# Kernel optimization log

Hardware: AMD Instinct MI355X
Metric: run time of the kernel (lower is better)

The kernel has to match this reference:

```python
import jax, jax.numpy as jnp
import numpy as np

NEG_SLOPE = 0.2
EPS = 1e-16  # PyG softmax denominator epsilon


def gat_conv(x, src, dst, W, a_src, a_dst, bias, concat):
    """PyG-style GATConv (eval mode, self-loops already included in src/dst)."""
    H, D = a_src.shape
    N = x.shape[0]
    h = (x @ W).reshape(N, H, D)                     # [N,H,D]
    alpha_s = jnp.einsum('nhd,hd->nh', h, a_src)     # [N,H]
    alpha_d = jnp.einsum('nhd,hd->nh', h, a_dst)     # [N,H]
    e = alpha_s[src] + alpha_d[dst]                  # [E,H]
    e = jax.nn.leaky_relu(e, NEG_SLOPE)
    # segment softmax over destination nodes
    m = jax.ops.segment_max(e, dst, num_segments=N)  # [N,H]
    m = jax.lax.stop_gradient(m)
    w = jnp.exp(e - m[dst])                          # [E,H]
    denom = jax.ops.segment_sum(w, dst, num_segments=N)  # [N,H]
    a = w / (denom[dst] + EPS)                       # [E,H]
    msg = h[src] * a[:, :, None]                     # [E,H,D]
    out = jax.ops.segment_sum(msg, dst, num_segments=N)  # [N,H,D]
    out = out.reshape(N, H * D) if concat else out.mean(axis=1)
    return out + bias


def setup_inputs() -> dict:
    key = jax.random.key(0)
    ks = jax.random.split(key, 10)
    N, E = 50000, 800000
    F_IN, H, D, C = 256, 4, 64, 64
    HID = H * D  # 256
    x = jax.random.normal(ks[0], (N, F_IN), dtype=jnp.float32)
    edge_index = jax.random.randint(ks[1], (2, E), 0, N, dtype=jnp.int64)
    g = 1.0 / np.sqrt(F_IN)
    W0 = jax.random.normal(ks[2], (F_IN, HID), dtype=jnp.float32) * g
    att_src0 = jax.random.normal(ks[3], (H, D), dtype=jnp.float32) * 0.1
    att_dst0 = jax.random.normal(ks[4], (H, D), dtype=jnp.float32) * 0.1
    b0 = jnp.zeros((HID,), dtype=jnp.float32)
    g2 = 1.0 / np.sqrt(HID)
    W1 = jax.random.normal(ks[5], (HID, C), dtype=jnp.float32) * g2
    att_src1 = jax.random.normal(ks[6], (1, C), dtype=jnp.float32) * 0.1
    att_dst1 = jax.random.normal(ks[7], (1, C), dtype=jnp.float32) * 0.1
    b1 = jnp.zeros((C,), dtype=jnp.float32)
    return {"x": x, "edge_index": edge_index, "W0": W0, "att_src0": att_src0,
            "att_dst0": att_dst0, "b0": b0, "W1": W1, "att_src1": att_src1,
            "att_dst1": att_dst1, "b1": b1}


def reference(x, edge_index, W0, att_src0, att_dst0, b0, W1, att_src1, att_dst1, b1):
    N = x.shape[0]
    loops = jnp.arange(N, dtype=edge_index.dtype)
    src = jnp.concatenate([edge_index[0], loops])  # add self-loops (PyG default)
    dst = jnp.concatenate([edge_index[1], loops])
    # layer 0: concat heads, then ELU (dropout is identity in eval mode)
    h = gat_conv(x, src, dst, W0, att_src0, att_dst0, b0, concat=True)
    h = jax.nn.elu(h)
    # layer 1: single head, no concat (mean over 1 head)
    out = gat_conv(h, src, dst, W1, att_src1, att_dst1, b1, concat=False)
    return out
```

## Files before the change

kernel.cpp:

```cpp
#include <hip/hip_runtime.h>
#include <hip/hip_bf16.h>
#include <math.h>


#define NEG_SLOPE 0.2f
#define CAP0 128
#define CAP1 128

typedef __attribute__((ext_vector_type(8))) short bf16x8;
typedef __attribute__((ext_vector_type(4))) float f32x4;

static __device__ __forceinline__ unsigned f2bf_rne(float f) {
  unsigned u = __float_as_uint(f);
  return (u + 0x7fffu + ((u >> 16) & 1u)) >> 16;
}
static __device__ __forceinline__ float bf2f(unsigned u16) {
  return __uint_as_float(u16 << 16);
}
static __device__ __forceinline__ void fma4(float4& acc, float w, uint2 v) {
  acc.x = fmaf(w, __uint_as_float(v.x << 16), acc.x);
  acc.y = fmaf(w, __uint_as_float(v.x & 0xffff0000u), acc.y);
  acc.z = fmaf(w, __uint_as_float(v.y << 16), acc.z);
  acc.w = fmaf(w, __uint_as_float(v.y & 0xffff0000u), acc.w);
}


__global__ void gat_cvt_bf16(const float* __restrict__ in,
                             ushort* __restrict__ out, int n8) {
  int i = blockIdx.x * blockDim.x + threadIdx.x;
  if (i >= n8) return;
  float4 a = *(const float4*)&in[(size_t)i * 8];
  float4 b = *(const float4*)&in[(size_t)i * 8 + 4];
  uint4 o;
  o.x = f2bf_rne(a.x) | (f2bf_rne(a.y) << 16);
  o.y = f2bf_rne(a.z) | (f2bf_rne(a.w) << 16);
  o.z = f2bf_rne(b.x) | (f2bf_rne(b.y) << 16);
  o.w = f2bf_rne(b.z) | (f2bf_rne(b.w) << 16);
  *(uint4*)&out[(size_t)i * 8] = o;
}

__global__ void gat_cvtT_bf16(const float* __restrict__ W,
                              ushort* __restrict__ Wt, int K, int Nw) {
  int i = blockIdx.x * blockDim.x + threadIdx.x;
  if (i >= K * Nw) return;
  int n = i / K, k = i - n * K;
  Wt[i] = (ushort)f2bf_rne(W[(size_t)k * Nw + n]);
}


__global__ void gat_count_kernel(const int* __restrict__ dst, int E, int N,
                                 int* __restrict__ counts) {
  int i = blockIdx.x * blockDim.x + threadIdx.x;
  int ET = E + N;
  if (i >= ET) return;
  int d = (i < E) ? dst[i] : (i - E);
  atomicAdd(&counts[d], 1);
}

__global__ __launch_bounds__(1024) void gat_scan_kernel(
    const int* __restrict__ counts, int* __restrict__ row_off,
    int* __restrict__ cursor, int n) {
  __shared__ int wsum[16];
  __shared__ int s_carry;
  int tid = threadIdx.x;
  int lane = tid & 63;
  int wid = tid >> 6;
  if (tid == 0) s_carry = 0;
  __syncthreads();
  const int TILE = 4096;
  for (int base = 0; base < n; base += TILE) {
    int idx = base + tid * 4;
    int4 v = {0, 0, 0, 0};
    if (idx + 3 < n) {
      v = *(const int4*)&counts[idx];
    } else {
      if (idx + 0 < n) v.x = counts[idx + 0];
      if (idx + 1 < n) v.y = counts[idx + 1];
      if (idx + 2 < n) v.z = counts[idx + 2];
      if (idx + 3 < n) v.w = counts[idx + 3];
    }
    int t0 = v.x, t1 = t0 + v.y, t2 = t1 + v.z, t3 = t2 + v.w;
    int x = t3;
    #pragma unroll
    for (int off = 1; off < 64; off <<= 1) {
      int y = __shfl_up(x, off, 64);
      if (lane >= off) x += y;
    }
    if (lane == 63) wsum[wid] = x;
    __syncthreads();
    if (tid < 16) {
      int s = wsum[tid];
      #pragma unroll
      for (int off = 1; off < 16; off <<= 1) {
        int y = __shfl_up(s, off, 16);
        if (tid >= off) s += y;
      }
      wsum[tid] = s;
    }
    __syncthreads();
    int carry = s_carry;
    int excl_wave = (wid > 0) ? wsum[wid - 1] : 0;
    int b = carry + excl_wave + (x - t3);
    if (idx + 0 < n) { row_off[idx + 0] = b;      cursor[idx + 0] = b;      }
    if (idx + 1 < n) { row_off[idx + 1] = b + t0; cursor[idx + 1] = b + t0; }
    if (idx + 2 < n) { row_off[idx + 2] = b + t1; cursor[idx + 2] = b + t1; }
    if (idx + 3 < n) { row_off[idx + 3] = b + t2; cursor[idx + 3] = b + t2; }
    __syncthreads();
    if (tid == 1023) s_carry = b + t3;
    __syncthreads();
  }
  if (threadIdx.x == 0) row_off[n] = s_carry;
}

__global__ void gat_fill_kernel(const int* __restrict__ src,
                                const int* __restrict__ dst, int E, int N,
                                int* __restrict__ cursor, int* __restrict__ col) {
  int i = blockIdx.x * blockDim.x + threadIdx.x;
  int ET = E + N;
  if (i >= ET) return;
  int s, d;
  if (i < E) { s = src[i]; d = dst[i]; }
  else       { s = d = i - E; }
  int pos = atomicAdd(&cursor[d], 1);
  col[pos] = s;
}


template <int BN, int WM, int WN, bool WRITE_F32, bool WRITE_BF16, bool ALPHA>
__global__ __launch_bounds__(256) void gat_gemm_bf16(
    const ushort* __restrict__ A, const ushort* __restrict__ Bt,
    float* __restrict__ C, ushort* __restrict__ Cb, int M, int K, int N,
    const float* __restrict__ a_src, const float* __restrict__ a_dst,
    float* __restrict__ as_out, float* __restrict__ ad_out, int H) {
  constexpr int BM = 128, BK = 32;
  constexpr int MR = WM / 16, NR = WN / 16;
  constexpr int WCOLS = BN / WN;
  __shared__ __align__(16) ushort Al[BM][40];
  __shared__ __align__(16) ushort Bl[BN][40];
  int tid = threadIdx.x;
  int lane = tid & 63, wid = tid >> 6;
  int wrow = (wid / WCOLS) * WM, wcol = (wid % WCOLS) * WN;
  int brow = blockIdx.x * BM, bcol = blockIdx.y * BN;
  int r0 = tid >> 2, seg = tid & 3;
  int kg = lane >> 4, rl = lane & 15;
  f32x4 acc[MR][NR] = {};
  for (int k0 = 0; k0 < K; k0 += BK) {
    #pragma unroll
    for (int h = 0; h < BM / 64; ++h) {
      int row = r0 + h * 64;
      int ar = brow + row;
      uint4 v = make_uint4(0u, 0u, 0u, 0u);
      if (ar < M) v = *(const uint4*)&A[(size_t)ar * K + k0 + seg * 8];
      *(uint4*)&Al[row][seg * 8] = v;
    }
    #pragma unroll
    for (int h = 0; h < BN / 64; ++h) {
      int row = r0 + h * 64;
      uint4 v = *(const uint4*)&Bt[(size_t)(bcol + row) * K + k0 + seg * 8];
      *(uint4*)&Bl[row][seg * 8] = v;
    }
    __syncthreads();
    bf16x8 af[MR], bfr[NR];
    #pragma unroll
    for (int m = 0; m < MR; ++m)
      af[m] = *(const bf16x8*)&Al[wrow + m * 16 + rl][kg * 8];
    #pragma unroll
    for (int n = 0; n < NR; ++n)
      bfr[n] = *(const bf16x8*)&Bl[wcol + n * 16 + rl][kg * 8];
    #pragma unroll
    for (int m = 0; m < MR; ++m)
      #pragma unroll
      for (int n = 0; n < NR; ++n)
        acc[m][n] = __builtin_amdgcn_mfma_f32_16x16x32_bf16(
            af[m], bfr[n], acc[m][n], 0, 0, 0);
    __syncthreads();
  }
  int orow = kg * 4;
  #pragma unroll
  for (int m = 0; m < MR; ++m) {
    #pragma unroll
    for (int j = 0; j < 4; ++j) {
      int r = brow + wrow + m * 16 + orow + j;
      if (r < M) {
        #pragma unroll
        for (int n = 0; n < NR; ++n) {
          int c = bcol + wcol + n * 16 + rl;
          float v = acc[m][n][j];
          if constexpr (WRITE_F32) C[(size_t)r * N + c] = v;
          if constexpr (WRITE_BF16) Cb[(size_t)r * N + c] = (ushort)f2bf_rne(v);
        }
      }
    }
  }
  if constexpr (ALPHA) {
    static_assert(WN == 64, "alpha fusion needs one head per wave");
    int hh = (bcol + wcol) >> 6;
    float asv[NR], adv[NR];
    #pragma unroll
    for (int n = 0; n < NR; ++n) {
      asv[n] = a_src[hh * 64 + n * 16 + rl];
      adv[n] = a_dst[hh * 64 + n * 16 + rl];
    }
    #pragma unroll
    for (int m = 0; m < MR; ++m) {
      #pragma unroll
      for (int j = 0; j < 4; ++j) {
        float ps = 0.f, pd = 0.f;
        #pragma unroll
        for (int n = 0; n < NR; ++n) {
          ps = fmaf(acc[m][n][j], asv[n], ps);
          pd = fmaf(acc[m][n][j], adv[n], pd);
        }
        #pragma unroll
        for (int off = 1; off < 16; off <<= 1) {
          ps += __shfl_xor(ps, off, 64);
          pd += __shfl_xor(pd, off, 64);
        }
        int r = brow + wrow + m * 16 + orow + j;
        if (rl == 0 && r < M) {
          as_out[(size_t)r * H + hh] = ps;
          ad_out[(size_t)r * H + hh] = pd;
        }
      }
    }
  }
}


__global__ __launch_bounds__(256) void gat_agg0_kernel(
    const unsigned* __restrict__ h0b, const float* __restrict__ as,
    const float* __restrict__ ad, const int* __restrict__ row_off,
    const int* __restrict__ col, const float* __restrict__ bias,
    ushort* __restrict__ x1b, int N) {
  __shared__ int scol[4][CAP0];
  __shared__ float wt[4][CAP0][4];
  int lane = threadIdx.x & 63;
  int wid = threadIdx.x >> 6;
  int n = blockIdx.x * 4 + wid;
  if (n >= N) return;
  int beg = row_off[n];
  int deg = row_off[n + 1] - beg;
  int degc = deg < CAP0 ? deg : CAP0;
  for (int jj = lane; jj < degc; jj += 64) scol[wid][jj] = col[beg + jj];

  int q = lane >> 4, slot = lane & 15;
  float adv = ad[n * 4 + q];

  float m = -INFINITY;
  for (int jj = slot; jj < deg; jj += 16) {
    int s = (jj < CAP0) ? scol[wid][jj] : col[beg + jj];
    float e = as[s * 4 + q] + adv;
    e = (e > 0.f) ? e : NEG_SLOPE * e;
    if (jj < CAP0) wt[wid][jj][q] = e;
    m = fmaxf(m, e);
  }
  #pragma unroll
  for (int off = 8; off; off >>= 1) m = fmaxf(m, __shfl_xor(m, off, 64));

  float dsum = 0.f;
  for (int jj = slot; jj < deg; jj += 16) {
    float e;
    if (jj < CAP0) {
      e = wt[wid][jj][q];
    } else {
      int s = col[beg + jj];
      e = as[s * 4 + q] + adv;
      e = (e > 0.f) ? e : NEG_SLOPE * e;
    }
    float w = __expf(e - m);
    if (jj < CAP0) wt[wid][jj][q] = w;
    dsum += w;
  }
  #pragma unroll
  for (int off = 8; off; off >>= 1) dsum += __shfl_xor(dsum, off, 64);
  float inv = 1.f / (dsum + 1e-16f);

  float4 acc = make_float4(0.f, 0.f, 0.f, 0.f);
  int c2 = lane * 2;
  if (deg <= CAP0) {
    int jj = 0;
    for (; jj + 8 <= deg; jj += 8) {
      int s0 = __builtin_amdgcn_readfirstlane(scol[wid][jj + 0]);
      int s1 = __builtin_amdgcn_readfirstlane(scol[wid][jj + 1]);
      int s2 = __builtin_amdgcn_readfirstlane(scol[wid][jj + 2]);
      int s3 = __builtin_amdgcn_readfirstlane(scol[wid][jj + 3]);
      int s4 = __builtin_amdgcn_readfirstlane(scol[wid][jj + 4]);
      int s5 = __builtin_amdgcn_readfirstlane(scol[wid][jj + 5]);
      int s6 = __builtin_amdgcn_readfirstlane(scol[wid][jj + 6]);
      int s7 = __builtin_amdgcn_readfirstlane(scol[wid][jj + 7]);
      uint2 v0 = *(const uint2*)(h0b + (size_t)s0 * 128 + c2);
      uint2 v1 = *(const uint2*)(h0b + (size_t)s1 * 128 + c2);
      uint2 v2 = *(const uint2*)(h0b + (size_t)s2 * 128 + c2);
      uint2 v3 = *(const uint2*)(h0b + (size_t)s3 * 128 + c2);
      uint2 v4 = *(const uint2*)(h0b + (size_t)s4 * 128 + c2);
      uint2 v5 = *(const uint2*)(h0b + (size_t)s5 * 128 + c2);
      uint2 v6 = *(const uint2*)(h0b + (size_t)s6 * 128 + c2);
      uint2 v7 = *(const uint2*)(h0b + (size_t)s7 * 128 + c2);
      float w0 = wt[wid][jj + 0][q];
      float w1 = wt[wid][jj + 1][q];
      float w2 = wt[wid][jj + 2][q];
      float w3 = wt[wid][jj + 3][q];
      float w4 = wt[wid][jj + 4][q];
      float w5 = wt[wid][jj + 5][q];
      float w6 = wt[wid][jj + 6][q];
      float w7 = wt[wid][jj + 7][q];
      fma4(acc, w0, v0); fma4(acc, w1, v1); fma4(acc, w2, v2); fma4(acc, w3, v3);
      fma4(acc, w4, v4); fma4(acc, w5, v5); fma4(acc, w6, v6); fma4(acc, w7, v7);
    }
    for (; jj < deg; ++jj) {
      int s = __builtin_amdgcn_readfirstlane(scol[wid][jj]);
      uint2 v = *(const uint2*)(h0b + (size_t)s * 128 + c2);
      fma4(acc, wt[wid][jj][q], v);
    }
  } else {
    for (int jj = 0; jj < deg; ++jj) {
      int s = (jj < CAP0) ? scol[wid][jj] : col[beg + jj];
      s = __builtin_amdgcn_readfirstlane(s);
      uint2 v = *(const uint2*)(h0b + (size_t)s * 128 + c2);
      float w;
      if (jj < CAP0) {
        w = wt[wid][jj][q];
      } else {
        float e = as[s * 4 + q] + adv;
        e = (e > 0.f) ? e : NEG_SLOPE * e;
        w = __expf(e - m);
      }
      fma4(acc, w, v);
    }
  }

  int c0 = lane * 4;
  float4 bv = *(const float4*)&bias[c0];
  float o0 = acc.x * inv + bv.x;
  float o1 = acc.y * inv + bv.y;
  float o2 = acc.z * inv + bv.z;
  float o3 = acc.w * inv + bv.w;
  o0 = (o0 > 0.f) ? o0 : (__expf(o0) - 1.f);
  o1 = (o1 > 0.f) ? o1 : (__expf(o1) - 1.f);
  o2 = (o2 > 0.f) ? o2 : (__expf(o2) - 1.f);
  o3 = (o3 > 0.f) ? o3 : (__expf(o3) - 1.f);
  uint2 p;
  p.x = f2bf_rne(o0) | (f2bf_rne(o1) << 16);
  p.y = f2bf_rne(o2) | (f2bf_rne(o3) << 16);
  *(uint2*)&x1b[(size_t)n * 256 + c0] = p;
}


__global__ __launch_bounds__(256) void gat_agg1_kernel(
    const ushort* __restrict__ h1b, const float* __restrict__ as,
    const float* __restrict__ ad, const int* __restrict__ row_off,
    const int* __restrict__ col, const float* __restrict__ bias,
    float* __restrict__ out, int N) {
  __shared__ int scol[4][CAP1];
  __shared__ float wt[4][CAP1];
  int lane = threadIdx.x & 63;
  int wid = threadIdx.x >> 6;
  int n = blockIdx.x * 4 + wid;
  if (n >= N) return;
  int beg = row_off[n];
  int deg = row_off[n + 1] - beg;
  int degc = deg < CAP1 ? deg : CAP1;
  for (int jj = lane; jj < degc; jj += 64) scol[wid][jj] = col[beg + jj];
  float adv = ad[n];

  float m = -INFINITY;
  for (int jj = lane; jj < deg; jj += 64) {
    int s = (jj < CAP1) ? scol[wid][jj] : col[beg + jj];
    float e = as[s] + adv;
    e = (e > 0.f) ? e : NEG_SLOPE * e;
    if (jj < CAP1) wt[wid][jj] = e;
    m = fmaxf(m, e);
  }
  #pragma unroll
  for (int off = 32; off; off >>= 1) m = fmaxf(m, __shfl_xor(m, off, 64));

  float dsum = 0.f;
  for (int jj = lane; jj < deg; jj += 64) {
    float e;
    if (jj < CAP1) {
      e = wt[wid][jj];
    } else {
      int s = col[beg + jj];
      e = as[s] + adv;
      e = (e > 0.f) ? e : NEG_SLOPE * e;
    }
    float w = __expf(e - m);
    if (jj < CAP1) wt[wid][jj] = w;
    dsum += w;
  }
  #pragma unroll
  for (int off = 32; off; off >>= 1) dsum += __shfl_xor(dsum, off, 64);
  float inv = 1.f / (dsum + 1e-16f);

  float acc = 0.f;
  if (deg <= CAP1) {
    int jj = 0;
    for (; jj + 8 <= deg; jj += 8) {
      int s0 = __builtin_amdgcn_readfirstlane(scol[wid][jj + 0]);
      int s1 = __builtin_amdgcn_readfirstlane(scol[wid][jj + 1]);
      int s2 = __builtin_amdgcn_readfirstlane(scol[wid][jj + 2]);
      int s3 = __builtin_amdgcn_readfirstlane(scol[wid][jj + 3]);
      int s4 = __builtin_amdgcn_readfirstlane(scol[wid][jj + 4]);
      int s5 = __builtin_amdgcn_readfirstlane(scol[wid][jj + 5]);
      int s6 = __builtin_amdgcn_readfirstlane(scol[wid][jj + 6]);
      int s7 = __builtin_amdgcn_readfirstlane(scol[wid][jj + 7]);
      float v0 = bf2f(h1b[(size_t)s0 * 64 + lane]);
      float v1 = bf2f(h1b[(size_t)s1 * 64 + lane]);
      float v2 = bf2f(h1b[(size_t)s2 * 64 + lane]);
      float v3 = bf2f(h1b[(size_t)s3 * 64 + lane]);
      float v4 = bf2f(h1b[(size_t)s4 * 64 + lane]);
      float v5 = bf2f(h1b[(size_t)s5 * 64 + lane]);
      float v6 = bf2f(h1b[(size_t)s6 * 64 + lane]);
      float v7 = bf2f(h1b[(size_t)s7 * 64 + lane]);
      acc = fmaf(wt[wid][jj + 0], v0, acc);
      acc = fmaf(wt[wid][jj + 1], v1, acc);
      acc = fmaf(wt[wid][jj + 2], v2, acc);
      acc = fmaf(wt[wid][jj + 3], v3, acc);
      acc = fmaf(wt[wid][jj + 4], v4, acc);
      acc = fmaf(wt[wid][jj + 5], v5, acc);
      acc = fmaf(wt[wid][jj + 6], v6, acc);
      acc = fmaf(wt[wid][jj + 7], v7, acc);
    }
    for (; jj < deg; ++jj) {
      int s = __builtin_amdgcn_readfirstlane(scol[wid][jj]);
      acc = fmaf(wt[wid][jj], bf2f(h1b[(size_t)s * 64 + lane]), acc);
    }
  } else {
    for (int jj = 0; jj < deg; ++jj) {
      int s = (jj < CAP1) ? scol[wid][jj] : col[beg + jj];
      s = __builtin_amdgcn_readfirstlane(s);
      float v = bf2f(h1b[(size_t)s * 64 + lane]);
      float w;
      if (jj < CAP1) {
        w = wt[wid][jj];
      } else {
        float e = as[s] + adv;
        e = (e > 0.f) ? e : NEG_SLOPE * e;
        w = __expf(e - m);
      }
      acc = fmaf(w, v, acc);
    }
  }
  out[(size_t)n * 64 + lane] = acc * inv + bias[lane];
}


extern "C" void kernel_launch(void* const* d_in, const int* in_sizes, int n_in,
                              void* d_out, int out_size, void* d_ws, size_t ws_size,
                              hipStream_t stream) {
  const float* x        = (const float*)d_in[0];
  const int*   eidx     = (const int*)d_in[1];
  const float* W0       = (const float*)d_in[2];
  const float* att_src0 = (const float*)d_in[3];
  const float* att_dst0 = (const float*)d_in[4];
  const float* b0       = (const float*)d_in[5];
  const float* W1       = (const float*)d_in[6];
  const float* att_src1 = (const float*)d_in[7];
  const float* att_dst1 = (const float*)d_in[8];
  const float* b1       = (const float*)d_in[9];
  float* out = (float*)d_out;

  const int F_IN = 256, HID = 256, H = 4, C = 64;
  const int N = in_sizes[0] / F_IN;
  const int E = in_sizes[1] / 2;
  const int ET = E + N;

  const int* src = eidx;
  const int* dst = eidx + E;

  char* w = (char*)d_ws;
  auto take = [&](size_t bytes) {
    char* p = w;
    w += (bytes + 255) & ~(size_t)255;
    return p;
  };
  ushort* xb      = (ushort*)take((size_t)N * F_IN * 2);
  ushort* W0t     = (ushort*)take((size_t)F_IN * HID * 2);
  ushort* W1t     = (ushort*)take((size_t)HID * C * 2);
  ushort* h0b     = (ushort*)take((size_t)N * HID * 2);
  ushort* x1b     = (ushort*)take((size_t)N * HID * 2);
  ushort* h1b     = (ushort*)take((size_t)N * C * 2);
  float*  as0     = (float*)take((size_t)N * H * 4);
  float*  ad0     = (float*)take((size_t)N * H * 4);
  float*  as1     = (float*)take((size_t)N * 4);
  float*  ad1     = (float*)take((size_t)N * 4);
  int*    row_off = (int*)take((size_t)(N + 1) * 4);
  int*    cursor  = (int*)take((size_t)N * 4);
  int*    counts  = (int*)take((size_t)N * 4);
  int*    col     = (int*)take((size_t)ET * 4);

  {
    int n8 = N * F_IN / 8;
    gat_cvt_bf16<<<(n8 + 255) / 256, 256, 0, stream>>>(x, xb, n8);
    gat_cvtT_bf16<<<(F_IN * HID + 255) / 256, 256, 0, stream>>>(W0, W0t, F_IN, HID);
    gat_cvtT_bf16<<<(HID * C + 255) / 256, 256, 0, stream>>>(W1, W1t, HID, C);
  }

  (void)hipMemsetAsync(counts, 0, (size_t)N * 4, stream);
  {
    int blocks = (ET + 255) / 256;
    gat_count_kernel<<<blocks, 256, 0, stream>>>(dst, E, N, counts);
    gat_scan_kernel<<<1, 1024, 0, stream>>>(counts, row_off, cursor, N);
    gat_fill_kernel<<<blocks, 256, 0, stream>>>(src, dst, E, N, cursor, col);
  }

  {
    dim3 grid((N + 127) / 128, HID / 128);
    gat_gemm_bf16<128, 64, 64, false, true, true>
        <<<grid, 256, 0, stream>>>(xb, W0t, nullptr, h0b, N, F_IN, HID,
                                   att_src0, att_dst0, as0, ad0, H);
  }
  gat_agg0_kernel<<<(N + 3) / 4, 256, 0, stream>>>((const unsigned*)h0b, as0,
                                                   ad0, row_off, col, b0, x1b, N);

  {
    dim3 grid((N + 127) / 128, C / 64);
    gat_gemm_bf16<64, 32, 64, false, true, true>
        <<<grid, 256, 0, stream>>>(x1b, W1t, nullptr, h1b, N, HID, C,
                                   att_src1, att_dst1, as1, ad1, 1);
  }
  gat_agg1_kernel<<<(N + 3) / 4, 256, 0, stream>>>(h1b, as1, ad1, row_off, col,
                                                   b1, out, N);
}
```

Measured before the change: 280.7 us.

## Fuse x-to-bf16 conversion into GEMM, widen layer-0 tile, retune aggregation loops

Drops the separate fp32-to-bf16 pass over x and instead converts A tiles while staging them in the first GEMM, saving one full read and write of the input. The layer-0 GEMM now uses 512-thread blocks covering all 256 output columns, so A is read once per row block. The layer-0 aggregation unroll goes from 8 to 4 neighbours. Layer-1 aggregation splits each wave into two halves that handle alternate edges with 2-wide bf16 loads and then combine them with a shuffle. The wider GEMM re-reads fp32 A directly and uses more LDS and registers per block, which may lower occupancy.

```diff
diff --git a/kernel.cpp b/kernel.cpp
--- a/kernel.cpp
+++ b/kernel.cpp
@@ -24,20 +24,6 @@
   acc.w = fmaf(w, __uint_as_float(v.y & 0xffff0000u), acc.w);
 }
 
-
-__global__ void gat_cvt_bf16(const float* __restrict__ in,
-                             ushort* __restrict__ out, int n8) {
-  int i = blockIdx.x * blockDim.x + threadIdx.x;
-  if (i >= n8) return;
-  float4 a = *(const float4*)&in[(size_t)i * 8];
-  float4 b = *(const float4*)&in[(size_t)i * 8 + 4];
-  uint4 o;
-  o.x = f2bf_rne(a.x) | (f2bf_rne(a.y) << 16);
-  o.y = f2bf_rne(a.z) | (f2bf_rne(a.w) << 16);
-  o.z = f2bf_rne(b.x) | (f2bf_rne(b.y) << 16);
-  o.w = f2bf_rne(b.z) | (f2bf_rne(b.w) << 16);
-  *(uint4*)&out[(size_t)i * 8] = o;
-}
 
 __global__ void gat_cvtT_bf16(const float* __restrict__ W,
                               ushort* __restrict__ Wt, int K, int Nw) {
@@ -126,15 +112,19 @@
 }
 
 
-template <int BN, int WM, int WN, bool WRITE_F32, bool WRITE_BF16, bool ALPHA>
-__global__ __launch_bounds__(256) void gat_gemm_bf16(
-    const ushort* __restrict__ A, const ushort* __restrict__ Bt,
-    float* __restrict__ C, ushort* __restrict__ Cb, int M, int K, int N,
-    const float* __restrict__ a_src, const float* __restrict__ a_dst,
+template <int THREADS, int BN, int WM, int WN, bool WRITE_BF16, bool ALPHA,
+          bool CVT_A>
+__global__ __launch_bounds__(THREADS) void gat_gemm_bf16(
+    const float* __restrict__ Af, const ushort* __restrict__ Ab,
+    const ushort* __restrict__ Bt, ushort* __restrict__ Cb, int M, int K,
+    int N, const float* __restrict__ a_src, const float* __restrict__ a_dst,
     float* __restrict__ as_out, float* __restrict__ ad_out, int H) {
   constexpr int BM = 128, BK = 32;
   constexpr int MR = WM / 16, NR = WN / 16;
   constexpr int WCOLS = BN / WN;
+  constexpr int RPP = THREADS / 4;
+  static_assert(BM % RPP == 0 && BN % RPP == 0, "staging");
+  static_assert((BM / WM) * (BN / WN) == THREADS / 64, "wave tiling");
   __shared__ __align__(16) ushort Al[BM][40];
   __shared__ __align__(16) ushort Bl[BN][40];
   int tid = threadIdx.x;
@@ -146,16 +136,27 @@
   f32x4 acc[MR][NR] = {};
   for (int k0 = 0; k0 < K; k0 += BK) {
     #pragma unroll
-    for (int h = 0; h < BM / 64; ++h) {
-      int row = r0 + h * 64;
+    for (int h = 0; h < BM / RPP; ++h) {
+      int row = r0 + h * RPP;
       int ar = brow + row;
       uint4 v = make_uint4(0u, 0u, 0u, 0u);
-      if (ar < M) v = *(const uint4*)&A[(size_t)ar * K + k0 + seg * 8];
+      if (ar < M) {
+        if constexpr (CVT_A) {
+          float4 a0 = *(const float4*)&Af[(size_t)ar * K + k0 + seg * 8];
+          float4 a1 = *(const float4*)&Af[(size_t)ar * K + k0 + seg * 8 + 4];
+          v.x = f2bf_rne(a0.x) | (f2bf_rne(a0.y) << 16);
+          v.y = f2bf_rne(a0.z) | (f2bf_rne(a0.w) << 16);
+          v.z = f2bf_rne(a1.x) | (f2bf_rne(a1.y) << 16);
+          v.w = f2bf_rne(a1.z) | (f2bf_rne(a1.w) << 16);
+        } else {
+          v = *(const uint4*)&Ab[(size_t)ar * K + k0 + seg * 8];
+        }
+      }
       *(uint4*)&Al[row][seg * 8] = v;
     }
     #pragma unroll
-    for (int h = 0; h < BN / 64; ++h) {
-      int row = r0 + h * 64;
+    for (int h = 0; h < BN / RPP; ++h) {
+      int row = r0 + h * RPP;
       uint4 v = *(const uint4*)&Bt[(size_t)(bcol + row) * K + k0 + seg * 8];
       *(uint4*)&Bl[row][seg * 8] = v;
     }
@@ -186,7 +187,6 @@
         for (int n = 0; n < NR; ++n) {
           int c = bcol + wcol + n * 16 + rl;
           float v = acc[m][n][j];
-          if constexpr (WRITE_F32) C[(size_t)r * N + c] = v;
           if constexpr (WRITE_BF16) Cb[(size_t)r * N + c] = (ushort)f2bf_rne(v);
         }
       }
@@ -279,33 +279,21 @@
   int c2 = lane * 2;
   if (deg <= CAP0) {
     int jj = 0;
-    for (; jj + 8 <= deg; jj += 8) {
+    for (; jj + 4 <= deg; jj += 4) {
       int s0 = __builtin_amdgcn_readfirstlane(scol[wid][jj + 0]);
       int s1 = __builtin_amdgcn_readfirstlane(scol[wid][jj + 1]);
       int s2 = __builtin_amdgcn_readfirstlane(scol[wid][jj + 2]);
       int s3 = __builtin_amdgcn_readfirstlane(scol[wid][jj + 3]);
-      int s4 = __builtin_amdgcn_readfirstlane(scol[wid][jj + 4]);
-      int s5 = __builtin_amdgcn_readfirstlane(scol[wid][jj + 5]);
-      int s6 = __builtin_amdgcn_readfirstlane(scol[wid][jj + 6]);
-      int s7 = __builtin_amdgcn_readfirstlane(scol[wid][jj + 7]);
       uint2 v0 = *(const uint2*)(h0b + (size_t)s0 * 128 + c2);
       uint2 v1 = *(const uint2*)(h0b + (size_t)s1 * 128 + c2);
       uint2 v2 = *(const uint2*)(h0b + (size_t)s2 * 128 + c2);
       uint2 v3 = *(const uint2*)(h0b + (size_t)s3 * 128 + c2);
-      uint2 v4 = *(const uint2*)(h0b + (size_t)s4 * 128 + c2);
-      uint2 v5 = *(const uint2*)(h0b + (size_t)s5 * 128 + c2);
-      uint2 v6 = *(const uint2*)(h0b + (size_t)s6 * 128 + c2);
-      uint2 v7 = *(const uint2*)(h0b + (size_t)s7 * 128 + c2);
       float w0 = wt[wid][jj + 0][q];
       float w1 = wt[wid][jj + 1][q];
       float w2 = wt[wid][jj + 2][q];
       float w3 = wt[wid][jj + 3][q];
-      float w4 = wt[wid][jj + 4][q];
-      float w5 = wt[wid][jj + 5][q];
-      float w6 = wt[wid][jj + 6][q];
-      float w7 = wt[wid][jj + 7][q];
-      fma4(acc, w0, v0); fma4(acc, w1, v1); fma4(acc, w2, v2); fma4(acc, w3, v3);
-      fma4(acc, w4, v4); fma4(acc, w5, v5); fma4(acc, w6, v6); fma4(acc, w7, v7);
+      fma4(acc, w0, v0); fma4(acc, w1, v1);
+      fma4(acc, w2, v2); fma4(acc, w3, v3);
     }
     for (; jj < deg; ++jj) {
       int s = __builtin_amdgcn_readfirstlane(scol[wid][jj]);
@@ -392,56 +380,79 @@
   for (int off = 32; off; off >>= 1) dsum += __shfl_xor(dsum, off, 64);
   float inv = 1.f / (dsum + 1e-16f);
 
-  float acc = 0.f;
+  int half = lane >> 5, c = lane & 31;
+  float ax = 0.f, ay = 0.f;
   if (deg <= CAP1) {
-    int jj = 0;
-    for (; jj + 8 <= deg; jj += 8) {
-      int s0 = __builtin_amdgcn_readfirstlane(scol[wid][jj + 0]);
-      int s1 = __builtin_amdgcn_readfirstlane(scol[wid][jj + 1]);
-      int s2 = __builtin_amdgcn_readfirstlane(scol[wid][jj + 2]);
-      int s3 = __builtin_amdgcn_readfirstlane(scol[wid][jj + 3]);
-      int s4 = __builtin_amdgcn_readfirstlane(scol[wid][jj + 4]);
-      int s5 = __builtin_amdgcn_readfirstlane(scol[wid][jj + 5]);
-      int s6 = __builtin_amdgcn_readfirstlane(scol[wid][jj + 6]);
-      int s7 = __builtin_amdgcn_readfirstlane(scol[wid][jj + 7]);
-      float v0 = bf2f(h1b[(size_t)s0 * 64 + lane]);
-      float v1 = bf2f(h1b[(size_t)s1 * 64 + lane]);
-      float v2 = bf2f(h1b[(size_t)s2 * 64 + lane]);
-      float v3 = bf2f(h1b[(size_t)s3 * 64 + lane]);
-      float v4 = bf2f(h1b[(size_t)s4 * 64 + lane]);
-      float v5 = bf2f(h1b[(size_t)s5 * 64 + lane]);
-      float v6 = bf2f(h1b[(size_t)s6 * 64 + lane]);
-      float v7 = bf2f(h1b[(size_t)s7 * 64 + lane]);
-      acc = fmaf(wt[wid][jj + 0], v0, acc);
-      acc = fmaf(wt[wid][jj + 1], v1, acc);
-      acc = fmaf(wt[wid][jj + 2], v2, acc);
-      acc = fmaf(wt[wid][jj + 3], v3, acc);
-      acc = fmaf(wt[wid][jj + 4], v4, acc);
-      acc = fmaf(wt[wid][jj + 5], v5, acc);
-      acc = fmaf(wt[wid][jj + 6], v6, acc);
-      acc = fmaf(wt[wid][jj + 7], v7, acc);
-    }
-    for (; jj < deg; ++jj) {
-      int s = __builtin_amdgcn_readfirstlane(scol[wid][jj]);
-      acc = fmaf(wt[wid][jj], bf2f(h1b[(size_t)s * 64 + lane]), acc);
+    int Pf = deg >> 1;
+    int t = 0;
+    for (; t + 4 <= Pf; t += 4) {
+      int j0 = 2 * t + half;
+      int s0 = scol[wid][j0 + 0];
+      int s1 = scol[wid][j0 + 2];
+      int s2 = scol[wid][j0 + 4];
+      int s3 = scol[wid][j0 + 6];
+      unsigned v0 = *(const unsigned*)(h1b + (size_t)s0 * 64 + c * 2);
+      unsigned v1 = *(const unsigned*)(h1b + (size_t)s1 * 64 + c * 2);
+      unsigned v2 = *(const unsigned*)(h1b + (size_t)s2 * 64 + c * 2);
+      unsigned v3 = *(const unsigned*)(h1b + (size_t)s3 * 64 + c * 2);
+      float w0 = wt[wid][j0 + 0];
+      float w1 = wt[wid][j0 + 2];
+      float w2 = wt[wid][j0 + 4];
+      float w3 = wt[wid][j0 + 6];
+      ax = fmaf(w0, bf2f(v0 & 0xffffu), ax);
+      ay = fmaf(w0, bf2f(v0 >> 16), ay);
+      ax = fmaf(w1, bf2f(v1 & 0xffffu), ax);
+      ay = fmaf(w1, bf2f(v1 >> 16), ay);
+      ax = fmaf(w2, bf2f(v2 & 0xffffu), ax);
+      ay = fmaf(w2, bf2f(v2 >> 16), ay);
+      ax = fmaf(w3, bf2f(v3 & 0xffffu), ax);
+      ay = fmaf(w3, bf2f(v3 >> 16), ay);
+    }
+    for (; t < Pf; ++t) {
+      int j0 = 2 * t + half;
+      int s = scol[wid][j0];
+      unsigned v = *(const unsigned*)(h1b + (size_t)s * 64 + c * 2);
+      float w = wt[wid][j0];
+      ax = fmaf(w, bf2f(v & 0xffffu), ax);
+      ay = fmaf(w, bf2f(v >> 16), ay);
+    }
+    if (deg & 1) {
+      int jj = deg - 1;
+      int s = scol[wid][jj];
+      unsigned v = *(const unsigned*)(h1b + (size_t)s * 64 + c * 2);
+      float w = (half == 0) ? wt[wid][jj] : 0.f;
+      ax = fmaf(w, bf2f(v & 0xffffu), ax);
+      ay = fmaf(w, bf2f(v >> 16), ay);
     }
   } else {
-    for (int jj = 0; jj < deg; ++jj) {
-      int s = (jj < CAP1) ? scol[wid][jj] : col[beg + jj];
-      s = __builtin_amdgcn_readfirstlane(s);
-      float v = bf2f(h1b[(size_t)s * 64 + lane]);
+    int P = (deg + 1) >> 1;
+    for (int t = 0; t < P; ++t) {
+      int jj = 2 * t + half;
+      int jc = jj < deg ? jj : (deg - 1);
+      int s = (jc < CAP1) ? scol[wid][jc] : col[beg + jc];
+      unsigned v = *(const unsigned*)(h1b + (size_t)s * 64 + c * 2);
       float w;
-      if (jj < CAP1) {
-        w = wt[wid][jj];
+      if (jc < CAP1) {
+        w = wt[wid][jc];
       } else {
         float e = as[s] + adv;
         e = (e > 0.f) ? e : NEG_SLOPE * e;
         w = __expf(e - m);
       }
-      acc = fmaf(w, v, acc);
-    }
-  }
-  out[(size_t)n * 64 + lane] = acc * inv + bias[lane];
+      if (jj >= deg) w = 0.f;
+      ax = fmaf(w, bf2f(v & 0xffffu), ax);
+      ay = fmaf(w, bf2f(v >> 16), ay);
+    }
+  }
+  ax += __shfl_xor(ax, 32, 64);
+  ay += __shfl_xor(ay, 32, 64);
+  if (half == 0) {
+    float2 bv = *(const float2*)&bias[c * 2];
+    float2 o;
+    o.x = ax * inv + bv.x;
+    o.y = ay * inv + bv.y;
+    *(float2*)&out[(size_t)n * 64 + c * 2] = o;
+  }
 }
 
 
@@ -474,7 +485,6 @@
     w += (bytes + 255) & ~(size_t)255;
     return p;
   };
-  ushort* xb      = (ushort*)take((size_t)N * F_IN * 2);
   ushort* W0t     = (ushort*)take((size_t)F_IN * HID * 2);
   ushort* W1t     = (ushort*)take((size_t)HID * C * 2);
   ushort* h0b     = (ushort*)take((size_t)N * HID * 2);
@@ -489,12 +499,8 @@
   int*    counts  = (int*)take((size_t)N * 4);
   int*    col     = (int*)take((size_t)ET * 4);
 
-  {
-    int n8 = N * F_IN / 8;
-    gat_cvt_bf16<<<(n8 + 255) / 256, 256, 0, stream>>>(x, xb, n8);
-    gat_cvtT_bf16<<<(F_IN * HID + 255) / 256, 256, 0, stream>>>(W0, W0t, F_IN, HID);
-    gat_cvtT_bf16<<<(HID * C + 255) / 256, 256, 0, stream>>>(W1, W1t, HID, C);
-  }
+  gat_cvtT_bf16<<<(F_IN * HID + 255) / 256, 256, 0, stream>>>(W0, W0t, F_IN, HID);
+  gat_cvtT_bf16<<<(HID * C + 255) / 256, 256, 0, stream>>>(W1, W1t, HID, C);
 
   (void)hipMemsetAsync(counts, 0, (size_t)N * 4, stream);
   {
@@ -505,9 +511,9 @@
   }
 
   {
-    dim3 grid((N + 127) / 128, HID / 128);
-    gat_gemm_bf16<128, 64, 64, false, true, true>
-        <<<grid, 256, 0, stream>>>(xb, W0t, nullptr, h0b, N, F_IN, HID,
+    dim3 grid((N + 127) / 128, HID / 256);
+    gat_gemm_bf16<512, 256, 64, 64, true, true, true>
+        <<<grid, 512, 0, stream>>>(x, nullptr, W0t, h0b, N, F_IN, HID,
                                    att_src0, att_dst0, as0, ad0, H);
   }
   gat_agg0_kernel<<<(N + 3) / 4, 256, 0, stream>>>((const unsigned*)h0b, as0,
@@ -515,8 +521,8 @@
 
   {
     dim3 grid((N + 127) / 128, C / 64);
-    gat_gemm_bf16<64, 32, 64, false, true, true>
-        <<<grid, 256, 0, stream>>>(x1b, W1t, nullptr, h1b, N, HID, C,
+    gat_gemm_bf16<256, 64, 32, 64, true, true, false>
+        <<<grid, 256, 0, stream>>>(nullptr, x1b, W1t, h1b, N, HID, C,
                                    att_src1, att_dst1, as1, ad1, 1);
   }
   gat_agg1_kernel<<<(N + 3) / 4, 256, 0, stream>>>(h1b, as1, ad1, row_off, col,
```

After: 266.6 us, median of 2. 5.0% less time.
